# Performance work log

Measured on AMD Instinct MI355X. Metric: run time of the kernel, lower is better.

The kernel has to match this reference:

```python
import jax, jax.numpy as jnp
import numpy as np

N = 30000      # points
E = 400000     # edges
CIN = 16       # input point features
B = 4          # graphs in batch
H, W = 60, 80  # BEV grid


def _mlp_params(key, cin, cout):
    k1, k2 = jax.random.split(key)
    wa = jax.random.normal(k1, (cin, cout), jnp.float32) * np.float32(np.sqrt(2.0 / cin))
    wb = jax.random.normal(k2, (cout, cout), jnp.float32) * np.float32(np.sqrt(2.0 / cout))
    return wa, jnp.zeros((cout,), jnp.float32), wb, jnp.zeros((cout,), jnp.float32)


def setup_inputs() -> dict:
    key = jax.random.key(0)
    ks = jax.random.split(key, 8)
    x = jax.random.normal(ks[0], (N, CIN), jnp.float32)
    r = jax.random.uniform(ks[1], (N, 3), jnp.float32)
    Z = 1.0 + 9.0 * r[:, 2]
    X = (r[:, 0] - 0.5) * 1.2 * Z   # |X/Z| < 0.6 -> mostly inside image
    Y = (r[:, 1] - 0.5) * 0.9 * Z
    pos = jnp.stack([X, Y, Z], axis=1)
    edge_index = jax.random.randint(ks[2], (2, E), 0, N, jnp.int32)
    batch = jnp.sort(jax.random.randint(ks[3], (N,), 0, B, jnp.int32))
    K = jnp.array([[500.0, 0.0, 320.0], [0.0, 500.0, 240.0], [0.0, 0.0, 1.0]], jnp.float32)
    w11, b11, w12, b12 = _mlp_params(ks[4], CIN + 3, 64)
    w21, b21, w22, b22 = _mlp_params(ks[5], 64 + 3, 128)
    w31, b31, w32, b32 = _mlp_params(ks[6], 128 + 3, 256)
    return dict(x=x, pos=pos, K=K,
                w11=w11, b11=b11, w12=w12, b12=b12,
                w21=w21, b21=b21, w22=w22, b22=b22,
                w31=w31, b31=b31, w32=w32, b32=b32,
                edge_index=edge_index, batch=batch)


def _mlp(h, wa, ba, wb, bb):
    return jax.nn.relu(h @ wa + ba) @ wb + bb


def _pointnet_conv(feat, rel, src, dst, wa, ba, wb, bb):
    # PyG PointNetConv: msg = local_nn([x_j, pos_j - pos_i]); max-aggregate at target i
    msg = _mlp(jnp.concatenate([feat[src], rel], axis=1), wa, ba, wb, bb)
    agg = jax.ops.segment_max(msg, dst, num_segments=N)
    return jnp.where(jnp.isfinite(agg), agg, 0.0)  # empty segments -> 0 (PyG fill)


def _points_to_image(feat, pos, batch, K):
    X, Y, Z = pos[:, 0], pos[:, 1], pos[:, 2]
    u = ((K[0, 0] * X / Z + K[0, 2]) / 640.0 * W).astype(jnp.int32)  # trunc like .long()
    v = ((K[1, 1] * Y / Z + K[1, 2]) / 480.0 * H).astype(jnp.int32)
    mask = (u >= 0) & (u < W) & (v >= 0) & (v < H)
    idx = jnp.where(mask, batch * (H * W) + v * W + u, 0)
    contrib = feat * mask[:, None].astype(feat.dtype)
    flat = jnp.zeros((B * H * W, feat.shape[1]), feat.dtype).at[idx].add(contrib)
    return flat.reshape(B, H, W, feat.shape[1]).transpose(0, 3, 1, 2)


def reference(x, pos, K, w11, b11, w12, b12, w21, b21, w22, b22, w31, b31, w32, b32,
              edge_index, batch):
    src, dst = edge_index[0], edge_index[1]
    rel = pos[src] - pos[dst]
    h = _pointnet_conv(x, rel, src, dst, w11, b11, w12, b12)
    h = _pointnet_conv(h, rel, src, dst, w21, b21, w22, b22)
    h = _pointnet_conv(h, rel, src, dst, w31, b31, w32, b32)
    return _points_to_image(h, pos, batch, K)  # [B, 256, H, W]
```

## Files before the change

kernel.cpp:

```cpp
#include <hip/hip_runtime.h>
#include <math.h>

#define NN 30000
#define NE 400000

typedef _Float16 f16;
typedef _Float16 f16x8 __attribute__((ext_vector_type(8)));
typedef _Float16 f16x4 __attribute__((ext_vector_type(4)));
typedef float f32x4 __attribute__((ext_vector_type(4)));

__device__ __forceinline__ void atomic_max_f(float* addr, float v) {
    if (v >= 0.0f) {
        atomicMax((int*)addr, __float_as_int(v));
    } else {
        atomicMin((unsigned int*)addr, __float_as_uint(v));
    }
}

__global__ __launch_bounds__(256) void fill_neg_inf(float* p, int n) {
    int i = blockIdx.x * blockDim.x + threadIdx.x;
    int stride = gridDim.x * blockDim.x;
    for (; i < n; i += stride) p[i] = -INFINITY;
}

__global__ __launch_bounds__(256) void hist_dst(const int* __restrict__ dst,
                                                int* __restrict__ counts) {
    int e = blockIdx.x * 256 + threadIdx.x;
    if (e < NE) atomicAdd(&counts[dst[e]], 1);
}

__global__ __launch_bounds__(1024) void scan_counts(const int* __restrict__ counts,
                                                    int* __restrict__ cursor) {
    __shared__ int lsum[1024];
    const int t = threadIdx.x;
    const int base = t * 30;
    int s = 0;
    for (int i = 0; i < 30; ++i) {
        int idx = base + i;
        if (idx < NN) s += counts[idx];
    }
    lsum[t] = s;
    __syncthreads();
    int acc = s;
    for (int off = 1; off < 1024; off <<= 1) {
        int v = (t >= off) ? lsum[t - off] : 0;
        __syncthreads();
        acc += v;
        lsum[t] = acc;
        __syncthreads();
    }
    int run = acc - s;
    for (int i = 0; i < 30; ++i) {
        int idx = base + i;
        if (idx < NN) { cursor[idx] = run; run += counts[idx]; }
    }
}

__global__ __launch_bounds__(256) void scatter_edges(const int* __restrict__ src,
                                                     const int* __restrict__ dst,
                                                     int* __restrict__ cursor,
                                                     int* __restrict__ srcS,
                                                     int* __restrict__ dstS) {
    int e = blockIdx.x * 256 + threadIdx.x;
    if (e >= NE) return;
    int d = dst[e];
    int p = atomicAdd(&cursor[d], 1);
    srcS[p] = src[e];
    dstS[p] = d;
}

template<int K, int N>
__global__ __launch_bounds__(256) void pack_w(const float* __restrict__ wsrc,
                                              f16* __restrict__ pB) {
    int f = blockIdx.x * 256 + threadIdx.x;
    if (f >= K * N) return;
    int j = f & 7;
    int l = (f >> 3) & 63;
    int rest = f >> 9;
    constexpr int KS = K / 32;
    int ks = rest % KS;
    int nt = rest / KS;
    int k = ks * 32 + ((l >> 4) << 3) + j;
    int n = nt * 16 + (l & 15);
    pB[f] = (f16)wsrc[k * N + n];
}

__global__ __launch_bounds__(256) void cast_f16(const float* __restrict__ w,
                                                f16* __restrict__ o, int n) {
    int i = blockIdx.x * 256 + threadIdx.x;
    if (i < n) o[i] = (f16)w[i];
}

template<int K, int COUT>
__global__ __launch_bounds__(256) void node_linear(const float* __restrict__ feat,
                                                   const float* __restrict__ wa,
                                                   const float* __restrict__ b,
                                                   f16* __restrict__ A) {
    constexpr int NPB = 8;
    constexpr int G   = 256 / COUT;
    constexpr int NPT = NPB / G;
    __shared__ float sf[NPB * K];
    const int node0 = blockIdx.x * NPB;
    for (int idx = threadIdx.x; idx < NPB * K; idx += 256) {
        float v = feat[node0 * K + idx];
        if (!isfinite(v)) v = 0.0f;
        sf[idx] = v;
    }
    __syncthreads();
    const int j  = threadIdx.x % COUT;
    const int g  = threadIdx.x / COUT;
    const int n0 = g * NPT;
    float acc[NPT];
#pragma unroll
    for (int i = 0; i < NPT; i++) acc[i] = 0.0f;
    for (int k = 0; k < K; k++) {
        float w = wa[k * COUT + j];
#pragma unroll
        for (int nn = 0; nn < NPT; nn++)
            acc[nn] = fmaf(sf[(n0 + nn) * K + k], w, acc[nn]);
    }
    const float bj = b[j];
#pragma unroll
    for (int nn = 0; nn < NPT; nn++)
        A[(size_t)(node0 + n0 + nn) * COUT + j] = (f16)(acc[nn] + bj);
}

template<int K, int C>
__global__ __launch_bounds__(256) void node_gemm(const float* __restrict__ feat,
                                                 const f16* __restrict__ pW,
                                                 const float* __restrict__ bias,
                                                 f16* __restrict__ A) {
    constexpr int NTW = C / 64;
    constexpr int KS  = K / 32;
    __shared__ __align__(16) unsigned char smem[64 * K * 2];
    const int tid = threadIdx.x;
    const int node0 = blockIdx.x * 64;

    {
        const int e = tid >> 2, p = tid & 3;
        const bool valid = (node0 + e) < NN;
        const float* frow = feat + (size_t)(node0 + e) * K;
#pragma unroll
        for (int ch = 0; ch < K / 32; ++ch) {
            const int j0 = (ch * 4 + p) * 8;
            f16x8 hv;
#pragma unroll
            for (int jj = 0; jj < 8; ++jj) {
                float v = valid ? frow[j0 + jj] : 0.0f;
                if (!isfinite(v)) v = 0.0f;
                hv[jj] = (f16)v;
            }
            *(f16x8*)(smem + e * (K * 2) + ((j0 * 2) ^ ((e & 7) << 4))) = hv;
        }
    }
    __syncthreads();

    const int w = tid >> 6, l = tid & 63, lr = l & 15, lg = l >> 4;
    f32x4 acc[4][NTW] = {};
#pragma unroll
    for (int ks = 0; ks < KS; ++ks) {
        f16x8 af[4];
#pragma unroll
        for (int m = 0; m < 4; ++m) {
            const int row = m * 16 + lr;
            af[m] = *(const f16x8*)(smem + row * (K * 2)
                     + (((ks * 32 + lg * 8) * 2) ^ ((row & 7) << 4)));
        }
#pragma unroll
        for (int nt = 0; nt < NTW; ++nt) {
            const int ntg = w * NTW + nt;
            f16x8 bf = *(const f16x8*)(pW + ((size_t)(ntg * KS + ks) * 64 + l) * 8);
#pragma unroll
            for (int m = 0; m < 4; ++m)
                acc[m][nt] = __builtin_amdgcn_mfma_f32_16x16x32_f16(af[m], bf, acc[m][nt], 0, 0, 0);
        }
    }
#pragma unroll
    for (int m = 0; m < 4; ++m)
#pragma unroll
        for (int nt = 0; nt < NTW; ++nt) {
            const int col = w * (C / 4) + nt * 16 + lr;
            const float bv = bias[col];
#pragma unroll
            for (int rr = 0; rr < 4; ++rr) {
                const int row = m * 16 + lg * 4 + rr;
                if (node0 + row < NN)
                    A[(size_t)(node0 + row) * C + col] = (f16)(acc[m][nt][rr] + bv);
            }
        }
}

template<int C, int NW>
__global__ __launch_bounds__(NW * 64, 4) void edge_mfma(const f16* __restrict__ Ah,
                                                        const f16* __restrict__ warelh,
                                                        const f16* __restrict__ pB,
                                                        const float* __restrict__ bb,
                                                        const float* __restrict__ pos,
                                                        const int* __restrict__ srcS,
                                                        const int* __restrict__ dstS,
                                                        float* __restrict__ agg) {
    constexpr int TE   = 64;
    constexpr int BLK  = NW * 64;
    constexpr int CW   = C / NW;
    constexpr int NTW  = CW / 16;
    constexpr int KS   = C / 32;
    constexpr int CPR  = C / 8;
    constexpr int LOGCPR = (C == 256) ? 5 : (C == 128 ? 4 : 3);
    static_assert(NTW >= 1, "geometry");

    __shared__ __align__(16) unsigned char h1[TE * C * 2];
    __shared__ __align__(16) f16 s_warel[3 * C];
    __shared__ __align__(8)  f16 s_rel[TE][4];
    __shared__ int s_src[TE], s_dst[TE];

    const int tid = threadIdx.x;
    const int nwg = gridDim.x;
    const int q8 = nwg >> 3, r8 = nwg & 7;
    const int xcd = blockIdx.x & 7, o = blockIdx.x >> 3;
    const int bid = (xcd < r8 ? xcd * (q8 + 1) : r8 * (q8 + 1) + (xcd - r8) * q8) + o;
    const int e0 = bid * TE;

    if (tid < TE) {
        int s = srcS[e0 + tid], d = dstS[e0 + tid];
        s_src[tid] = s; s_dst[tid] = d;
        s_rel[tid][0] = (f16)(pos[3 * s + 0] - pos[3 * d + 0]);
        s_rel[tid][1] = (f16)(pos[3 * s + 1] - pos[3 * d + 1]);
        s_rel[tid][2] = (f16)(pos[3 * s + 2] - pos[3 * d + 2]);
        s_rel[tid][3] = (f16)0.f;
    }
    for (int i = tid; i < 3 * C / 8; i += BLK)
        ((f16x8*)s_warel)[i] = ((const f16x8*)warelh)[i];
    __syncthreads();

#pragma unroll
    for (int i = 0; i < (8 * C) / BLK; ++i) {
        const int g    = i * BLK + tid;
        const int row  = g >> LOGCPR;
        const int slot = g & (CPR - 1);
        const int s = s_src[row];
        const f16x4 rl = *(const f16x4*)&s_rel[row][0];
        const f16 rx = rl[0], ry = rl[1], rz = rl[2];
        const f16x8 rxv = {rx, rx, rx, rx, rx, rx, rx, rx};
        const f16x8 ryv = {ry, ry, ry, ry, ry, ry, ry, ry};
        const f16x8 rzv = {rz, rz, rz, rz, rz, rz, rz, rz};
        f16x8 av = *(const f16x8*)(Ah + (size_t)s * C + slot * 8);
        const f16* wp = s_warel + slot * 8;
        f16x8 w0 = *(const f16x8*)(wp);
        f16x8 w1 = *(const f16x8*)(wp + C);
        f16x8 w2 = *(const f16x8*)(wp + 2 * C);
        f16x8 hv = av + rxv * w0 + ryv * w1 + rzv * w2;
#pragma unroll
        for (int jj = 0; jj < 8; ++jj)
            hv[jj] = hv[jj] > (f16)0.f ? hv[jj] : (f16)0.f;
        *(f16x8*)(h1 + row * (2 * C) + ((slot * 16) ^ ((row & 7) << 4))) = hv;
    }
    __syncthreads();

    const int w = tid >> 6, l = tid & 63, lr = l & 15, lg = l >> 4;
    f32x4 acc[4][NTW] = {};
#pragma unroll
    for (int ks = 0; ks < KS; ++ks) {
        f16x8 af[4];
#pragma unroll
        for (int m = 0; m < 4; ++m) {
            const int row = m * 16 + lr;
            af[m] = *(const f16x8*)(h1 + row * (2 * C)
                     + (((ks * 32 + lg * 8) * 2) ^ ((row & 7) << 4)));
        }
#pragma unroll
        for (int nt = 0; nt < NTW; ++nt) {
            f16x8 bf = *(const f16x8*)(pB + ((size_t)((w * NTW + nt) * KS + ks) * 64 + l) * 8);
#pragma unroll
            for (int m = 0; m < 4; ++m)
                acc[m][nt] = __builtin_amdgcn_mfma_f32_16x16x32_f16(af[m], bf, acc[m][nt], 0, 0, 0);
        }
    }

    float bbv[NTW];
#pragma unroll
    for (int nt = 0; nt < NTW; ++nt) bbv[nt] = bb[w * CW + nt * 16 + lr];

    const int myd = s_dst[l];
    const int pd  = s_dst[l == 0 ? 0 : l - 1];
    unsigned long long m = __ballot((l == 0) || (myd != pd));

    while (m) {
        const int a = __builtin_ctzll(m);
        const unsigned long long m2 = m & (m - 1);
        const int b = m2 ? __builtin_ctzll(m2) : 64;
        m = m2;
        const int d = s_dst[a];
#pragma unroll
        for (int nt = 0; nt < NTW; ++nt) {
            float v = -INFINITY;
#pragma unroll
            for (int mm = 0; mm < 4; ++mm) {
                if (b <= mm * 16 || a >= mm * 16 + 16) continue;
#pragma unroll
                for (int rr = 0; rr < 4; ++rr) {
                    const int row = mm * 16 + lg * 4 + rr;
                    const bool in = (row >= a) && (row < b);
                    v = fmaxf(v, in ? acc[mm][nt][rr] : -INFINITY);
                }
            }
            v = fmaxf(v, __shfl_xor(v, 16, 64));
            v = fmaxf(v, __shfl_xor(v, 32, 64));
            if (lg == 0)
                atomic_max_f(&agg[(size_t)d * C + w * CW + nt * 16 + lr], v + bbv[nt]);
        }
    }
}

__global__ __launch_bounds__(256) void scatter_img(const float* __restrict__ feat,
                                                   const float* __restrict__ pos,
                                                   const float* __restrict__ Km,
                                                   const int* __restrict__ batch,
                                                   float* __restrict__ img) {
    const int n = blockIdx.x;
    const float X = pos[3 * n + 0], Y = pos[3 * n + 1], Z = pos[3 * n + 2];
    const float k00 = Km[0], k02 = Km[2], k11 = Km[4], k12 = Km[5];
    const int u = (int)((k00 * X / Z + k02) / 640.0f * 80.0f);
    const int v = (int)((k11 * Y / Z + k12) / 480.0f * 60.0f);
    if (u < 0 || u >= 80 || v < 0 || v >= 60) return;
    const int p = (batch[n] * 60 + v) * 80 + u;
    const int c = threadIdx.x;
    float val = feat[(size_t)n * 256 + c];
    if (!isfinite(val)) val = 0.0f;
    atomicAdd(img + (size_t)p * 256 + c, val);
}

__global__ __launch_bounds__(256) void transpose_img(const float* __restrict__ img,
                                                     float* __restrict__ out) {
    __shared__ float tile[32][33];
    const int b = blockIdx.z;
    const int p0 = blockIdx.x * 32, c0 = blockIdx.y * 32;
    const float* src = img + (size_t)b * 4800 * 256;
    float* dst = out + (size_t)b * 256 * 4800;
    const int tx = threadIdx.x & 31, ty = threadIdx.x >> 5;
#pragma unroll
    for (int i = 0; i < 32; i += 8)
        tile[ty + i][tx] = src[(size_t)(p0 + ty + i) * 256 + c0 + tx];
    __syncthreads();
#pragma unroll
    for (int i = 0; i < 32; i += 8)
        dst[(size_t)(c0 + ty + i) * 4800 + p0 + tx] = tile[tx][ty + i];
}

extern "C" void kernel_launch(void* const* d_in, const int* in_sizes, int n_in,
                              void* d_out, int out_size, void* d_ws, size_t ws_size,
                              hipStream_t stream) {
    const float* x   = (const float*)d_in[0];
    const float* pos = (const float*)d_in[1];
    const float* Km  = (const float*)d_in[2];
    const float* w11 = (const float*)d_in[3];
    const float* b11 = (const float*)d_in[4];
    const float* w12 = (const float*)d_in[5];
    const float* b12 = (const float*)d_in[6];
    const float* w21 = (const float*)d_in[7];
    const float* b21 = (const float*)d_in[8];
    const float* w22 = (const float*)d_in[9];
    const float* b22 = (const float*)d_in[10];
    const float* w31 = (const float*)d_in[11];
    const float* b31 = (const float*)d_in[12];
    const float* w32 = (const float*)d_in[13];
    const float* b32 = (const float*)d_in[14];
    const int* edge  = (const int*)d_in[15];
    const int* batch = (const int*)d_in[16];
    const int* srcp = edge;
    const int* dstp = edge + NE;
    float* out = (float*)d_out;

    float* aggA  = (float*)d_ws;
    float* aggB  = aggA + (size_t)NN * 256;
    f16*   Ah    = (f16*)(aggB + (size_t)NN * 256);
    int*   srcS  = (int*)(Ah + (size_t)NN * 256);
    int*   dstS  = srcS + NE;
    int*   counts = dstS + NE;
    int*   cursor = counts + NN;
    f16*   pW1   = (f16*)(cursor + NN);
    f16*   pW2   = pW1 + 64 * 64;
    f16*   pW3   = pW2 + 128 * 128;
    f16*   pW2n  = pW3 + 256 * 256;
    f16*   pW3n  = pW2n + 64 * 128;
    f16*   wr1   = pW3n + 128 * 256;
    f16*   wr2   = wr1 + 3 * 64;
    f16*   wr3   = wr2 + 3 * 128;

    hipMemsetAsync(counts, 0, NN * sizeof(int), stream);
    hist_dst<<<(NE + 255) / 256, 256, 0, stream>>>(dstp, counts);
    scan_counts<<<1, 1024, 0, stream>>>(counts, cursor);
    scatter_edges<<<(NE + 255) / 256, 256, 0, stream>>>(srcp, dstp, cursor, srcS, dstS);

    pack_w<64, 64><<<(64 * 64 + 255) / 256, 256, 0, stream>>>(w12, pW1);
    pack_w<128, 128><<<(128 * 128 + 255) / 256, 256, 0, stream>>>(w22, pW2);
    pack_w<256, 256><<<(256 * 256 + 255) / 256, 256, 0, stream>>>(w32, pW3);
    pack_w<64, 128><<<(64 * 128 + 255) / 256, 256, 0, stream>>>(w21, pW2n);
    pack_w<128, 256><<<(128 * 256 + 255) / 256, 256, 0, stream>>>(w31, pW3n);
    cast_f16<<<1, 256, 0, stream>>>(w11 + 16 * 64, wr1, 3 * 64);
    cast_f16<<<2, 256, 0, stream>>>(w21 + 64 * 128, wr2, 3 * 128);
    cast_f16<<<3, 256, 0, stream>>>(w31 + 128 * 256, wr3, 3 * 256);

    node_linear<16, 64><<<NN / 8, 256, 0, stream>>>(x, w11, b11, Ah);
    fill_neg_inf<<<512, 256, 0, stream>>>(aggB, NN * 64);
    edge_mfma<64, 4><<<NE / 64, 256, 0, stream>>>(Ah, wr1, pW1, b12,
                                                  pos, srcS, dstS, aggB);
    node_gemm<64, 128><<<(NN + 63) / 64, 256, 0, stream>>>(aggB, pW2n, b21, Ah);
    fill_neg_inf<<<512, 256, 0, stream>>>(aggA, NN * 128);
    edge_mfma<128, 8><<<NE / 64, 512, 0, stream>>>(Ah, wr2, pW2, b22,
                                                   pos, srcS, dstS, aggA);
    node_gemm<128, 256><<<(NN + 63) / 64, 256, 0, stream>>>(aggA, pW3n, b31, Ah);
    fill_neg_inf<<<512, 256, 0, stream>>>(aggB, NN * 256);
    edge_mfma<256, 8><<<NE / 64, 512, 0, stream>>>(Ah, wr3, pW3, b32,
                                                   pos, srcS, dstS, aggB);
    hipMemsetAsync(aggA, 0, (size_t)4 * 4800 * 256 * sizeof(float), stream);
    scatter_img<<<NN, 256, 0, stream>>>(aggB, pos, Km, batch, aggA);
    transpose_img<<<dim3(150, 8, 4), 256, 0, stream>>>(aggA, out);
}
```

Before: 382.5 us.

## Enlarge edge tiles, prefetch weights, use plain stores for interior segments, batch scatter

The edge MFMA kernel now handles 128 edges per block. Each wave owns a 64-row by 32-column tile, and the block size grows to C*4 threads. B-fragment loads are double-buffered across k-steps. Destination segments that lie entirely inside a wave's 64 sorted edges are written with plain stores instead of atomic max. Separately, the -inf fill uses float4 stores and scatter_img processes 8 points per block. The larger tiles cut block count and atomic traffic, but 1024-thread blocks and doubled shared memory may reduce occupancy.

New measurement: 382.5 us. No clear change (+0.0%).

```diff
diff --git a/kernel.cpp b/kernel.cpp
--- a/kernel.cpp
+++ b/kernel.cpp
@@ -17,10 +17,11 @@
     }
 }
 
-__global__ __launch_bounds__(256) void fill_neg_inf(float* p, int n) {
+__global__ __launch_bounds__(256) void fill_neg_inf4(float4* p, int n4) {
     int i = blockIdx.x * blockDim.x + threadIdx.x;
     int stride = gridDim.x * blockDim.x;
-    for (; i < n; i += stride) p[i] = -INFINITY;
+    const float4 v = {-INFINITY, -INFINITY, -INFINITY, -INFINITY};
+    for (; i < n4; i += stride) p[i] = v;
 }
 
 __global__ __launch_bounds__(256) void hist_dst(const int* __restrict__ dst,
@@ -190,23 +191,21 @@
         }
 }
 
-template<int C, int NW>
-__global__ __launch_bounds__(NW * 64, 4) void edge_mfma(const f16* __restrict__ Ah,
-                                                        const f16* __restrict__ warelh,
-                                                        const f16* __restrict__ pB,
-                                                        const float* __restrict__ bb,
-                                                        const float* __restrict__ pos,
-                                                        const int* __restrict__ srcS,
-                                                        const int* __restrict__ dstS,
-                                                        float* __restrict__ agg) {
-    constexpr int TE   = 64;
-    constexpr int BLK  = NW * 64;
-    constexpr int CW   = C / NW;
-    constexpr int NTW  = CW / 16;
+template<int C>
+__global__ __launch_bounds__(C * 4, 4) void edge_mfma(const f16* __restrict__ Ah,
+                                                      const f16* __restrict__ warelh,
+                                                      const f16* __restrict__ pB,
+                                                      const float* __restrict__ bb,
+                                                      const float* __restrict__ pos,
+                                                      const int* __restrict__ srcS,
+                                                      const int* __restrict__ dstS,
+                                                      float* __restrict__ agg) {
+    constexpr int TE   = 128;
+    constexpr int BLK  = C * 4;
+    constexpr int CG   = C / 32;
     constexpr int KS   = C / 32;
     constexpr int CPR  = C / 8;
     constexpr int LOGCPR = (C == 256) ? 5 : (C == 128 ? 4 : 3);
-    static_assert(NTW >= 1, "geometry");
 
     __shared__ __align__(16) unsigned char h1[TE * C * 2];
     __shared__ __align__(16) f16 s_warel[3 * C];
@@ -233,7 +232,7 @@
     __syncthreads();
 
 #pragma unroll
-    for (int i = 0; i < (8 * C) / BLK; ++i) {
+    for (int i = 0; i < 4; ++i) {
         const int g    = i * BLK + tid;
         const int row  = g >> LOGCPR;
         const int slot = g & (CPR - 1);
@@ -257,31 +256,40 @@
     __syncthreads();
 
     const int w = tid >> 6, l = tid & 63, lr = l & 15, lg = l >> 4;
-    f32x4 acc[4][NTW] = {};
+    const int rg = w / CG, cg = w % CG;
+    const int rowoff = rg * 64;
+    f32x4 acc[4][2] = {};
+    f16x8 bfc[2], bfn[2];
+#pragma unroll
+    for (int nt = 0; nt < 2; ++nt)
+        bfc[nt] = *(const f16x8*)(pB + ((size_t)((cg * 2 + nt) * KS) * 64 + l) * 8);
 #pragma unroll
     for (int ks = 0; ks < KS; ++ks) {
+        if (ks + 1 < KS) {
+#pragma unroll
+            for (int nt = 0; nt < 2; ++nt)
+                bfn[nt] = *(const f16x8*)(pB + ((size_t)((cg * 2 + nt) * KS + ks + 1) * 64 + l) * 8);
+        }
         f16x8 af[4];
 #pragma unroll
         for (int m = 0; m < 4; ++m) {
-            const int row = m * 16 + lr;
+            const int row = rowoff + m * 16 + lr;
             af[m] = *(const f16x8*)(h1 + row * (2 * C)
                      + (((ks * 32 + lg * 8) * 2) ^ ((row & 7) << 4)));
         }
 #pragma unroll
-        for (int nt = 0; nt < NTW; ++nt) {
-            f16x8 bf = *(const f16x8*)(pB + ((size_t)((w * NTW + nt) * KS + ks) * 64 + l) * 8);
+        for (int nt = 0; nt < 2; ++nt)
 #pragma unroll
             for (int m = 0; m < 4; ++m)
-                acc[m][nt] = __builtin_amdgcn_mfma_f32_16x16x32_f16(af[m], bf, acc[m][nt], 0, 0, 0);
-        }
-    }
-
-    float bbv[NTW];
-#pragma unroll
-    for (int nt = 0; nt < NTW; ++nt) bbv[nt] = bb[w * CW + nt * 16 + lr];
-
-    const int myd = s_dst[l];
-    const int pd  = s_dst[l == 0 ? 0 : l - 1];
+                acc[m][nt] = __builtin_amdgcn_mfma_f32_16x16x32_f16(af[m], bfc[nt], acc[m][nt], 0, 0, 0);
+#pragma unroll
+        for (int nt = 0; nt < 2; ++nt) bfc[nt] = bfn[nt];
+    }
+
+    float bbv[2] = {bb[cg * 32 + lr], bb[cg * 32 + 16 + lr]};
+
+    const int myd = s_dst[rowoff + l];
+    const int pd  = s_dst[rowoff + (l == 0 ? 0 : l - 1)];
     unsigned long long m = __ballot((l == 0) || (myd != pd));
 
     while (m) {
@@ -289,9 +297,10 @@
         const unsigned long long m2 = m & (m - 1);
         const int b = m2 ? __builtin_ctzll(m2) : 64;
         m = m2;
-        const int d = s_dst[a];
-#pragma unroll
-        for (int nt = 0; nt < NTW; ++nt) {
+        const int d = s_dst[rowoff + a];
+        const bool interior = (a > 0) && (b < 64);
+#pragma unroll
+        for (int nt = 0; nt < 2; ++nt) {
             float v = -INFINITY;
 #pragma unroll
             for (int mm = 0; mm < 4; ++mm) {
@@ -305,8 +314,11 @@
             }
             v = fmaxf(v, __shfl_xor(v, 16, 64));
             v = fmaxf(v, __shfl_xor(v, 32, 64));
-            if (lg == 0)
-                atomic_max_f(&agg[(size_t)d * C + w * CW + nt * 16 + lr], v + bbv[nt]);
+            if (lg == 0) {
+                float* addr = &agg[(size_t)d * C + cg * 32 + nt * 16 + lr];
+                if (interior) *addr = v + bbv[nt];
+                else          atomic_max_f(addr, v + bbv[nt]);
+            }
         }
     }
 }
@@ -316,17 +328,21 @@
                                                    const float* __restrict__ Km,
                                                    const int* __restrict__ batch,
                                                    float* __restrict__ img) {
-    const int n = blockIdx.x;
-    const float X = pos[3 * n + 0], Y = pos[3 * n + 1], Z = pos[3 * n + 2];
+    const int n0 = blockIdx.x * 8;
+    const int c = threadIdx.x;
     const float k00 = Km[0], k02 = Km[2], k11 = Km[4], k12 = Km[5];
-    const int u = (int)((k00 * X / Z + k02) / 640.0f * 80.0f);
-    const int v = (int)((k11 * Y / Z + k12) / 480.0f * 60.0f);
-    if (u < 0 || u >= 80 || v < 0 || v >= 60) return;
-    const int p = (batch[n] * 60 + v) * 80 + u;
-    const int c = threadIdx.x;
-    float val = feat[(size_t)n * 256 + c];
-    if (!isfinite(val)) val = 0.0f;
-    atomicAdd(img + (size_t)p * 256 + c, val);
+#pragma unroll
+    for (int k = 0; k < 8; ++k) {
+        const int n = n0 + k;
+        const float X = pos[3 * n + 0], Y = pos[3 * n + 1], Z = pos[3 * n + 2];
+        const int u = (int)((k00 * X / Z + k02) / 640.0f * 80.0f);
+        const int v = (int)((k11 * Y / Z + k12) / 480.0f * 60.0f);
+        if (u < 0 || u >= 80 || v < 0 || v >= 60) continue;
+        const int p = (batch[n] * 60 + v) * 80 + u;
+        float val = feat[(size_t)n * 256 + c];
+        if (!isfinite(val)) val = 0.0f;
+        atomicAdd(img + (size_t)p * 256 + c, val);
+    }
 }
 
 __global__ __launch_bounds__(256) void transpose_img(const float* __restrict__ img,
@@ -401,18 +417,18 @@
     cast_f16<<<3, 256, 0, stream>>>(w31 + 128 * 256, wr3, 3 * 256);
 
     node_linear<16, 64><<<NN / 8, 256, 0, stream>>>(x, w11, b11, Ah);
-    fill_neg_inf<<<512, 256, 0, stream>>>(aggB, NN * 64);
-    edge_mfma<64, 4><<<NE / 64, 256, 0, stream>>>(Ah, wr1, pW1, b12,
+    fill_neg_inf4<<<512, 256, 0, stream>>>((float4*)aggB, NN * 64 / 4);
+    edge_mfma<64><<<NE / 128, 256, 0, stream>>>(Ah, wr1, pW1, b12,
+                                                pos, srcS, dstS, aggB);
+    node_gemm<64, 128><<<(NN + 63) / 64, 256, 0, stream>>>(aggB, pW2n, b21, Ah);
+    fill_neg_inf4<<<512, 256, 0, stream>>>((float4*)aggA, NN * 128 / 4);
+    edge_mfma<128><<<NE / 128, 512, 0, stream>>>(Ah, wr2, pW2, b22,
+                                                 pos, srcS, dstS, aggA);
+    node_gemm<128, 256><<<(NN + 63) / 64, 256, 0, stream>>>(aggA, pW3n, b31, Ah);
+    fill_neg_inf4<<<512, 256, 0, stream>>>((float4*)aggB, NN * 256 / 4);
+    edge_mfma<256><<<NE / 128, 1024, 0, stream>>>(Ah, wr3, pW3, b32,
                                                   pos, srcS, dstS, aggB);
-    node_gemm<64, 128><<<(NN + 63) / 64, 256, 0, stream>>>(aggB, pW2n, b21, Ah);
-    fill_neg_inf<<<512, 256, 0, stream>>>(aggA, NN * 128);
-    edge_mfma<128, 8><<<NE / 64, 512, 0, stream>>>(Ah, wr2, pW2, b22,
-                                                   pos, srcS, dstS, aggA);
-    node_gemm<128, 256><<<(NN + 63) / 64, 256, 0, stream>>>(aggA, pW3n, b31, Ah);
-    fill_neg_inf<<<512, 256, 0, stream>>>(aggB, NN * 256);
-    edge_mfma<256, 8><<<NE / 64, 512, 0, stream>>>(Ah, wr3, pW3, b32,
-                                                   pos, srcS, dstS, aggB);
     hipMemsetAsync(aggA, 0, (size_t)4 * 4800 * 256 * sizeof(float), stream);
-    scatter_img<<<NN, 256, 0, stream>>>(aggB, pos, Km, batch, aggA);
+    scatter_img<<<NN / 8, 256, 0, stream>>>(aggB, pos, Km, batch, aggA);
     transpose_img<<<dim3(150, 8, 4), 256, 0, stream>>>(aggA, out);
 }
```

## Prefetch gathered features, plain stores for interior segments, vectorize fills, batch scatter

Applied to the files above, without the earlier changes.

Several independent changes. The edge kernel now loads source indices and gathered node features into registers before the first barrier, with a two-deep prefetch, so gather latency overlaps the rel/weight setup. MFMA priority is raised during the GEMM loop. Destination segments that lie wholly inside a tile (edges are sorted by dst) are written with plain stores instead of atomic max. Separately, the -inf fill uses float4 stores and scatter_img handles 8 points per block. The plain-store path relies on each interior segment being owned by exactly one block; more registers in flight may lower occupancy.

Result: no change. 381.1 us (-0.4%).

```diff
diff --git a/kernel.cpp b/kernel.cpp
--- a/kernel.cpp
+++ b/kernel.cpp
@@ -17,10 +17,11 @@
     }
 }
 
-__global__ __launch_bounds__(256) void fill_neg_inf(float* p, int n) {
+__global__ __launch_bounds__(256) void fill_neg_inf4(float4* p, int n4) {
     int i = blockIdx.x * blockDim.x + threadIdx.x;
     int stride = gridDim.x * blockDim.x;
-    for (; i < n; i += stride) p[i] = -INFINITY;
+    const float4 v = {-INFINITY, -INFINITY, -INFINITY, -INFINITY};
+    for (; i < n4; i += stride) p[i] = v;
 }
 
 __global__ __launch_bounds__(256) void hist_dst(const int* __restrict__ dst,
@@ -206,12 +207,13 @@
     constexpr int KS   = C / 32;
     constexpr int CPR  = C / 8;
     constexpr int LOGCPR = (C == 256) ? 5 : (C == 128 ? 4 : 3);
-    static_assert(NTW >= 1, "geometry");
+    constexpr int CH   = (TE * CPR) / BLK;
+    static_assert(NTW >= 1 && CH >= 2, "geometry");
 
     __shared__ __align__(16) unsigned char h1[TE * C * 2];
     __shared__ __align__(16) f16 s_warel[3 * C];
     __shared__ __align__(8)  f16 s_rel[TE][4];
-    __shared__ int s_src[TE], s_dst[TE];
+    __shared__ int s_dst[TE];
 
     const int tid = threadIdx.x;
     const int nwg = gridDim.x;
@@ -220,9 +222,18 @@
     const int bid = (xcd < r8 ? xcd * (q8 + 1) : r8 * (q8 + 1) + (xcd - r8) * q8) + o;
     const int e0 = bid * TE;
 
+    const int slot = tid & (CPR - 1);
+    int sv[CH];
+    f16x8 av[CH];
+#pragma unroll
+    for (int i = 0; i < CH; ++i)
+        sv[i] = srcS[e0 + ((i * BLK + tid) >> LOGCPR)];
+    av[0] = *(const f16x8*)(Ah + (size_t)sv[0] * C + slot * 8);
+    av[1] = *(const f16x8*)(Ah + (size_t)sv[1] * C + slot * 8);
+
     if (tid < TE) {
         int s = srcS[e0 + tid], d = dstS[e0 + tid];
-        s_src[tid] = s; s_dst[tid] = d;
+        s_dst[tid] = d;
         s_rel[tid][0] = (f16)(pos[3 * s + 0] - pos[3 * d + 0]);
         s_rel[tid][1] = (f16)(pos[3 * s + 1] - pos[3 * d + 1]);
         s_rel[tid][2] = (f16)(pos[3 * s + 2] - pos[3 * d + 2]);
@@ -232,32 +243,33 @@
         ((f16x8*)s_warel)[i] = ((const f16x8*)warelh)[i];
     __syncthreads();
 
-#pragma unroll
-    for (int i = 0; i < (8 * C) / BLK; ++i) {
-        const int g    = i * BLK + tid;
-        const int row  = g >> LOGCPR;
-        const int slot = g & (CPR - 1);
-        const int s = s_src[row];
-        const f16x4 rl = *(const f16x4*)&s_rel[row][0];
-        const f16 rx = rl[0], ry = rl[1], rz = rl[2];
-        const f16x8 rxv = {rx, rx, rx, rx, rx, rx, rx, rx};
-        const f16x8 ryv = {ry, ry, ry, ry, ry, ry, ry, ry};
-        const f16x8 rzv = {rz, rz, rz, rz, rz, rz, rz, rz};
-        f16x8 av = *(const f16x8*)(Ah + (size_t)s * C + slot * 8);
+    {
         const f16* wp = s_warel + slot * 8;
-        f16x8 w0 = *(const f16x8*)(wp);
-        f16x8 w1 = *(const f16x8*)(wp + C);
-        f16x8 w2 = *(const f16x8*)(wp + 2 * C);
-        f16x8 hv = av + rxv * w0 + ryv * w1 + rzv * w2;
-#pragma unroll
-        for (int jj = 0; jj < 8; ++jj)
-            hv[jj] = hv[jj] > (f16)0.f ? hv[jj] : (f16)0.f;
-        *(f16x8*)(h1 + row * (2 * C) + ((slot * 16) ^ ((row & 7) << 4))) = hv;
+        const f16x8 w0 = *(const f16x8*)(wp);
+        const f16x8 w1 = *(const f16x8*)(wp + C);
+        const f16x8 w2 = *(const f16x8*)(wp + 2 * C);
+#pragma unroll
+        for (int i = 0; i < CH; ++i) {
+            if (i + 2 < CH)
+                av[i + 2] = *(const f16x8*)(Ah + (size_t)sv[i + 2] * C + slot * 8);
+            const int row = (i * BLK + tid) >> LOGCPR;
+            const f16x4 rl = *(const f16x4*)&s_rel[row][0];
+            const f16 rx = rl[0], ry = rl[1], rz = rl[2];
+            const f16x8 rxv = {rx, rx, rx, rx, rx, rx, rx, rx};
+            const f16x8 ryv = {ry, ry, ry, ry, ry, ry, ry, ry};
+            const f16x8 rzv = {rz, rz, rz, rz, rz, rz, rz, rz};
+            f16x8 hv = av[i] + rxv * w0 + ryv * w1 + rzv * w2;
+#pragma unroll
+            for (int jj = 0; jj < 8; ++jj)
+                hv[jj] = hv[jj] > (f16)0.f ? hv[jj] : (f16)0.f;
+            *(f16x8*)(h1 + row * (2 * C) + ((slot * 16) ^ ((row & 7) << 4))) = hv;
+        }
     }
     __syncthreads();
 
     const int w = tid >> 6, l = tid & 63, lr = l & 15, lg = l >> 4;
     f32x4 acc[4][NTW] = {};
+    __builtin_amdgcn_s_setprio(1);
 #pragma unroll
     for (int ks = 0; ks < KS; ++ks) {
         f16x8 af[4];
@@ -275,6 +287,7 @@
                 acc[m][nt] = __builtin_amdgcn_mfma_f32_16x16x32_f16(af[m], bf, acc[m][nt], 0, 0, 0);
         }
     }
+    __builtin_amdgcn_s_setprio(0);
 
     float bbv[NTW];
 #pragma unroll
@@ -290,6 +303,7 @@
         const int b = m2 ? __builtin_ctzll(m2) : 64;
         m = m2;
         const int d = s_dst[a];
+        const bool interior = (a > 0) && (b < 64);
 #pragma unroll
         for (int nt = 0; nt < NTW; ++nt) {
             float v = -INFINITY;
@@ -305,8 +319,11 @@
             }
             v = fmaxf(v, __shfl_xor(v, 16, 64));
             v = fmaxf(v, __shfl_xor(v, 32, 64));
-            if (lg == 0)
-                atomic_max_f(&agg[(size_t)d * C + w * CW + nt * 16 + lr], v + bbv[nt]);
+            if (lg == 0) {
+                float* addr = &agg[(size_t)d * C + w * CW + nt * 16 + lr];
+                if (interior) *addr = v + bbv[nt];
+                else          atomic_max_f(addr, v + bbv[nt]);
+            }
         }
     }
 }
@@ -316,17 +333,21 @@
                                                    const float* __restrict__ Km,
                                                    const int* __restrict__ batch,
                                                    float* __restrict__ img) {
-    const int n = blockIdx.x;
-    const float X = pos[3 * n + 0], Y = pos[3 * n + 1], Z = pos[3 * n + 2];
+    const int n0 = blockIdx.x * 8;
+    const int c = threadIdx.x;
     const float k00 = Km[0], k02 = Km[2], k11 = Km[4], k12 = Km[5];
-    const int u = (int)((k00 * X / Z + k02) / 640.0f * 80.0f);
-    const int v = (int)((k11 * Y / Z + k12) / 480.0f * 60.0f);
-    if (u < 0 || u >= 80 || v < 0 || v >= 60) return;
-    const int p = (batch[n] * 60 + v) * 80 + u;
-    const int c = threadIdx.x;
-    float val = feat[(size_t)n * 256 + c];
-    if (!isfinite(val)) val = 0.0f;
-    atomicAdd(img + (size_t)p * 256 + c, val);
+#pragma unroll
+    for (int k = 0; k < 8; ++k) {
+        const int n = n0 + k;
+        const float X = pos[3 * n + 0], Y = pos[3 * n + 1], Z = pos[3 * n + 2];
+        const int u = (int)((k00 * X / Z + k02) / 640.0f * 80.0f);
+        const int v = (int)((k11 * Y / Z + k12) / 480.0f * 60.0f);
+        if (u < 0 || u >= 80 || v < 0 || v >= 60) continue;
+        const int p = (batch[n] * 60 + v) * 80 + u;
+        float val = feat[(size_t)n * 256 + c];
+        if (!isfinite(val)) val = 0.0f;
+        atomicAdd(img + (size_t)p * 256 + c, val);
+    }
 }
 
 __global__ __launch_bounds__(256) void transpose_img(const float* __restrict__ img,
@@ -401,18 +422,18 @@
     cast_f16<<<3, 256, 0, stream>>>(w31 + 128 * 256, wr3, 3 * 256);
 
     node_linear<16, 64><<<NN / 8, 256, 0, stream>>>(x, w11, b11, Ah);
-    fill_neg_inf<<<512, 256, 0, stream>>>(aggB, NN * 64);
+    fill_neg_inf4<<<512, 256, 0, stream>>>((float4*)aggB, NN * 64 / 4);
     edge_mfma<64, 4><<<NE / 64, 256, 0, stream>>>(Ah, wr1, pW1, b12,
                                                   pos, srcS, dstS, aggB);
     node_gemm<64, 128><<<(NN + 63) / 64, 256, 0, stream>>>(aggB, pW2n, b21, Ah);
-    fill_neg_inf<<<512, 256, 0, stream>>>(aggA, NN * 128);
+    fill_neg_inf4<<<512, 256, 0, stream>>>((float4*)aggA, NN * 128 / 4);
     edge_mfma<128, 8><<<NE / 64, 512, 0, stream>>>(Ah, wr2, pW2, b22,
                                                    pos, srcS, dstS, aggA);
     node_gemm<128, 256><<<(NN + 63) / 64, 256, 0, stream>>>(aggA, pW3n, b31, Ah);
-    fill_neg_inf<<<512, 256, 0, stream>>>(aggB, NN * 256);
+    fill_neg_inf4<<<512, 256, 0, stream>>>((float4*)aggB, NN * 256 / 4);
     edge_mfma<256, 8><<<NE / 64, 512, 0, stream>>>(Ah, wr3, pW3, b32,
                                                    pos, srcS, dstS, aggB);
     hipMemsetAsync(aggA, 0, (size_t)4 * 4800 * 256 * sizeof(float), stream);
-    scatter_img<<<NN, 256, 0, stream>>>(aggB, pos, Km, batch, aggA);
+    scatter_img<<<NN / 8, 256, 0, stream>>>(aggB, pos, Km, batch, aggA);
     transpose_img<<<dim3(150, 8, 4), 256, 0, stream>>>(aggA, out);
 }
```
